# Kernel tuning notes

Measured on AMD Instinct MI355X. Metric: run time of the kernel, lower is better.

The kernel has to match this reference:

```python
import jax, jax.numpy as jnp
import numpy as np

# dims
Z, P, N, H = 16, 4, 466, 86          # z_dim, p_dim, n_dim, gmean(466,16)
B_SZ, T = 2048, 32                   # batch, number of eval times
INNER = 16                           # fixed trial-step budget per eval interval
ATOL, RTOL = 1e-20, 1e-5
H2B, H3B = 64, 2048                  # B-net hiddens: int(sqrt(16**3)), 16**3//2

# Dormand-Prince 5(4) tableau
A21 = 1/5
A31, A32 = 3/40, 9/40
A41, A42, A43 = 44/45, -56/15, 32/9
A51, A52, A53, A54 = 19372/6561, -25360/2187, 64448/6561, -212/729
A61, A62, A63, A64, A65 = 9017/3168, -355/33, 46732/5247, 49/176, -5103/18656
B1, B3, B4, B5, B6 = 35/384, 500/1113, 125/192, -2187/6784, 11/84
E1, E3, E4, E5, E6, E7 = 71/57600, -71/16695, 71/1920, -17253/339200, 22/525, -1/40


def _leaky(x):
    return jnp.where(x >= 0, x, 0.2 * x)


def setup_inputs() -> dict:
    key = jax.random.key(0)
    ks = jax.random.split(key, 26)
    w = lambda k, shape: (jax.random.normal(k, shape) * 0.05).astype(jnp.float32)
    inp = {}
    inp['n_0'] = jax.random.normal(ks[0], (B_SZ, N), dtype=jnp.float32)
    inp['p'] = jax.random.uniform(ks[1], (P,), dtype=jnp.float32)
    inp['tstep'] = jnp.arange(T, dtype=jnp.float32) / (T - 1)
    # autoencoder
    inp['We1'], inp['be1'] = w(ks[2], (N, H)), w(ks[3], (H,))
    inp['We2'], inp['be2'] = w(ks[4], (H, Z)), w(ks[5], (Z,))
    inp['Wd1'], inp['bd1'] = w(ks[6], (Z, H)), w(ks[7], (H,))
    inp['Wd2'], inp['bd2'] = w(ks[8], (H, N)), w(ks[9], (N,))
    # A net: P -> Z -> Z*Z//2 -> Z*Z
    inp['Wa1'], inp['ba1'] = w(ks[10], (P, Z)), w(ks[11], (Z,))
    inp['Wa2'], inp['ba2'] = w(ks[12], (Z, Z*Z//2)), w(ks[13], (Z*Z//2,))
    inp['Wa3'], inp['ba3'] = w(ks[14], (Z*Z//2, Z*Z)), w(ks[15], (Z*Z,))
    # B net: P -> Z -> 64 -> 2048 -> Z**3
    inp['Wb1'], inp['bb1'] = w(ks[16], (P, Z)), w(ks[17], (Z,))
    inp['Wb2'], inp['bb2'] = w(ks[18], (Z, H2B)), w(ks[19], (H2B,))
    inp['Wb3'], inp['bb3'] = w(ks[20], (H2B, H3B)), w(ks[21], (H3B,))
    inp['Wb4'], inp['bb4'] = w(ks[22], (H3B, Z**3)), w(ks[23], (Z**3,))
    return inp


def _solve(z0, tstep, Amat, Bten):
    # adaptive Dopri5 with integral (I) step-size controller; fixed trial budget per interval
    def f(z):  # g(z,p): A z + B z z
        return z @ Amat.T + jnp.einsum('ijk,bj,bk->bi', Bten, z, z)

    def step(y, dt):
        k1 = f(y)
        k2 = f(y + dt * (A21 * k1))
        k3 = f(y + dt * (A31 * k1 + A32 * k2))
        k4 = f(y + dt * (A41 * k1 + A42 * k2 + A43 * k3))
        k5 = f(y + dt * (A51 * k1 + A52 * k2 + A53 * k3 + A54 * k4))
        k6 = f(y + dt * (A61 * k1 + A62 * k2 + A63 * k3 + A64 * k4 + A65 * k5))
        y5 = y + dt * (B1 * k1 + B3 * k3 + B4 * k4 + B5 * k5 + B6 * k6)
        k7 = f(y5)
        err = dt * (E1 * k1 + E3 * k3 + E4 * k4 + E5 * k5 + E6 * k6 + E7 * k7)
        return y5, err

    def interval(carry, tpair):
        y, dt = carry
        t0, t1 = tpair[0], tpair[1]

        def inner(c, _):
            t, y, dt = c
            done = t >= t1 - 1e-10
            dtc = jnp.where(done, 0.0, jnp.minimum(dt, t1 - t))  # clip to interval end
            ynew, err = step(y, dtc)
            tol = ATOL + RTOL * jnp.maximum(jnp.abs(y), jnp.abs(ynew))
            en = jnp.sqrt(jnp.mean((err / tol) ** 2))
            accept = (en <= 1.0) & (~done)
            t = jnp.where(accept, t + dtc, t)
            y = jnp.where(accept, ynew, y)
            factor = jnp.clip(0.9 * jnp.maximum(en, 1e-12) ** -0.2, 0.2, 10.0)
            dt = jnp.where(done, dt, dt * factor)
            return (t, y, dt), None

        (tf, yf, dtf), _ = jax.lax.scan(inner, (t0, y, dt), None, length=INNER)
        return (yf, dtf), yf

    dt0 = (tstep[1] - tstep[0]) * 0.3
    tpairs = jnp.stack([tstep[:-1], tstep[1:]], axis=1)  # [T-1, 2]
    (_, _), ys = jax.lax.scan(interval, (z0, dt0), tpairs)
    return jnp.concatenate([z0[None], ys], axis=0)  # [T, b, Z]


def reference(n_0, p, tstep, We1, be1, We2, be2, Wd1, bd1, Wd2, bd2,
              Wa1, ba1, Wa2, ba2, Wa3, ba3,
              Wb1, bb1, Wb2, bb2, Wb3, bb3, Wb4, bb4):
    # encoder
    z0 = _leaky(n_0 @ We1 + be1) @ We2 + be2  # [b, Z]
    # A(p), B(p) depend only on p -> computed once per solve
    ha = _leaky(p @ Wa1 + ba1)
    ha = _leaky(ha @ Wa2 + ba2)
    Amat = _leaky(ha @ Wa3 + ba3).reshape(Z, Z)
    hb = _leaky(p @ Wb1 + bb1)
    hb = _leaky(hb @ Wb2 + bb2)
    hb = _leaky(hb @ Wb3 + bb3)
    Bten = _leaky(hb @ Wb4 + bb4).reshape(Z, Z, Z)
    zs = _solve(z0, tstep, Amat, Bten)  # [T, b, Z]
    # decoder
    return _leaky(zs @ Wd1 + bd1) @ Wd2 + bd2  # [T, b, N]
```

## Files before the change

### kernel.cpp

```cpp
#include <hip/hip_runtime.h>
#include <cmath>

#define DEV __device__ __forceinline__

static DEV float leakyf(float x){ return x >= 0.0f ? x : 0.2f*x; }

typedef float v2f __attribute__((ext_vector_type(2)));

constexpr float cA21 = (float)(1.0/5.0);
constexpr float cA31 = (float)(3.0/40.0),  cA32 = (float)(9.0/40.0);
constexpr float cA41 = (float)(44.0/45.0), cA42 = (float)(-56.0/15.0), cA43 = (float)(32.0/9.0);
constexpr float cA51 = (float)(19372.0/6561.0), cA52 = (float)(-25360.0/2187.0);
constexpr float cA53 = (float)(64448.0/6561.0), cA54 = (float)(-212.0/729.0);
constexpr float cA61 = (float)(9017.0/3168.0),  cA62 = (float)(-355.0/33.0);
constexpr float cA63 = (float)(46732.0/5247.0), cA64 = (float)(49.0/176.0);
constexpr float cA65 = (float)(-5103.0/18656.0);
constexpr float cB1 = (float)(35.0/384.0),  cB3 = (float)(500.0/1113.0), cB4 = (float)(125.0/192.0);
constexpr float cB5 = (float)(-2187.0/6784.0), cB6 = (float)(11.0/84.0);
constexpr float cE1 = (float)(71.0/57600.0), cE3 = (float)(-71.0/16695.0), cE4 = (float)(71.0/1920.0);
constexpr float cE5 = (float)(-17253.0/339200.0), cE6 = (float)(22.0/525.0), cE7 = (float)(-1.0/40.0);

#define WS_AMAT   0
#define WS_HB3    256
#define WS_BTEN   2304
#define WS_ZS     6400
#define WS_SLOTSF (6400 + 1048576)

__global__ void __launch_bounds__(256) k_smallnets(
    const float* __restrict__ p,
    const float* __restrict__ Wa1, const float* __restrict__ ba1,
    const float* __restrict__ Wa2, const float* __restrict__ ba2,
    const float* __restrict__ Wa3, const float* __restrict__ ba3,
    const float* __restrict__ Wb1, const float* __restrict__ bb1,
    const float* __restrict__ Wb2, const float* __restrict__ bb2,
    const float* __restrict__ Wb3, const float* __restrict__ bb3,
    float* __restrict__ wsf)
{
    __shared__ float sp[4], sa1[16], sa2[128], sb1[16], sb2[64];
    int tid = threadIdx.x;
    if (tid < 4) sp[tid] = p[tid];
    __syncthreads();
    if (tid < 16) {
        float a = ba1[tid];
        for (int j = 0; j < 4; ++j) a = fmaf(sp[j], Wa1[j*16+tid], a);
        sa1[tid] = leakyf(a);
        float c = bb1[tid];
        for (int j = 0; j < 4; ++j) c = fmaf(sp[j], Wb1[j*16+tid], c);
        sb1[tid] = leakyf(c);
    }
    __syncthreads();
    if (tid < 128) {
        float a = ba2[tid];
        for (int j = 0; j < 16; ++j) a = fmaf(sa1[j], Wa2[j*128+tid], a);
        sa2[tid] = leakyf(a);
    }
    if (tid < 64) {
        float c = bb2[tid];
        for (int j = 0; j < 16; ++j) c = fmaf(sb1[j], Wb2[j*64+tid], c);
        sb2[tid] = leakyf(c);
    }
    __syncthreads();
    {
        float a = ba3[tid];
        for (int j = 0; j < 128; ++j) a = fmaf(sa2[j], Wa3[j*256+tid], a);
        wsf[WS_AMAT + tid] = leakyf(a);
    }
    for (int q = 0; q < 8; ++q) {
        int o = q*256 + tid;
        float c = bb3[o];
        for (int j = 0; j < 64; ++j) c = fmaf(sb2[j], Wb3[j*2048+o], c);
        wsf[WS_HB3 + o] = leakyf(c);
    }
}

__global__ void __launch_bounds__(256) k_bten(
    const float* __restrict__ Wb4, const float* __restrict__ bb4, float* __restrict__ wsf)
{
    __shared__ float red[256];
    const float* hb3 = wsf + WS_HB3;
    float* Bten = wsf + WS_BTEN;
    int tid = threadIdx.x;
    int ol = tid & 15, part = tid >> 4;
    int o = blockIdx.x * 16 + ol;
    float a = 0.0f;
    for (int q = 0; q < 128; ++q) {
        int hh = part*128 + q;
        a = fmaf(hb3[hh], Wb4[(size_t)hh*4096 + o], a);
    }
    red[part*16 + ol] = a;
    __syncthreads();
    for (int s = 8; s >= 1; s >>= 1) {
        if (part < s) red[part*16+ol] += red[(part+s)*16+ol];
        __syncthreads();
    }
    if (tid < 16) {
        float v = red[tid] + bb4[blockIdx.x*16 + tid];
        Bten[blockIdx.x*16 + tid] = leakyf(v);
    }
}

__global__ void __launch_bounds__(256) k_encoder(
    const float* __restrict__ n0,
    const float* __restrict__ We1, const float* __restrict__ be1,
    const float* __restrict__ We2, const float* __restrict__ be2,
    float* __restrict__ zs)
{
    __shared__ float hL[8][88];
    int tid = threadIdx.x;
    int r = tid >> 5, c = tid & 31;
    int row = blockIdx.x * 8 + r;
    const float* nrow = n0 + (size_t)row * 466;
    int c2 = (c + 64 < 86) ? (c + 64) : 85;
    float a0 = 0.f, a1 = 0.f, a2 = 0.f;
    for (int n = 0; n < 466; ++n) {
        float nv = nrow[n];
        a0 = fmaf(nv, We1[n*86 + c], a0);
        a1 = fmaf(nv, We1[n*86 + c + 32], a1);
        a2 = fmaf(nv, We1[n*86 + c2], a2);
    }
    hL[r][c]      = leakyf(a0 + be1[c]);
    hL[r][c + 32] = leakyf(a1 + be1[c + 32]);
    if (c < 22) hL[r][c + 64] = leakyf(a2 + be1[c + 64]);
    __syncthreads();
    if (tid < 128) {
        int r2 = tid >> 4, ii = tid & 15;
        int row2 = blockIdx.x * 8 + r2;
        float a = be2[ii];
        #pragma unroll
        for (int hh = 0; hh < 86; ++hh) a = fmaf(hL[r2][hh], We2[hh*16 + ii], a);
        zs[(size_t)row2 * 16 + ii] = a;
    }
}

__global__ void __launch_bounds__(256) k_solver(
    const float* __restrict__ tstep, float* __restrict__ wsf)
{
    __shared__ float zL[8][16];
    __shared__ float redA[2][4], redB[2][4];
    float* Amat = wsf + WS_AMAT;
    float* Bten = wsf + WS_BTEN;
    float* zs   = wsf + WS_ZS;
    unsigned long long* slots = (unsigned long long*)(wsf + WS_SLOTSF);

    const int tid = threadIdx.x, blk = blockIdx.x;
    const int e = tid >> 5, g = tid & 31;
    const int i = g >> 1, h = g & 1, h8 = h * 8;
    const int b = blk * 8 + e;

    v2f Bl2[64], aR2[8];
    #pragma unroll
    for (int p = 0; p < 8; ++p) {
        int jA = (h8 + 2*p)     & 15;
        int jB = (h8 + 2*p + 1) & 15;
        v2f ap; ap.x = (h == 0) ? Amat[i*16 + 2*p] : 0.0f;
        ap.y = (h == 0) ? Amat[i*16 + 2*p + 1] : 0.0f;
        aR2[p] = ap;
        const float4* bpA = (const float4*)(Bten + i*256 + jA*16 + h8);
        const float4* bpB = (const float4*)(Bten + i*256 + jB*16 + h8);
        float4 a0 = bpA[0], a1 = bpA[1], b0 = bpB[0], b1 = bpB[1];
        v2f q;
        q.x=a0.x; q.y=b0.x; Bl2[p*8+0]=q;  q.x=a0.y; q.y=b0.y; Bl2[p*8+1]=q;
        q.x=a0.z; q.y=b0.z; Bl2[p*8+2]=q;  q.x=a0.w; q.y=b0.w; Bl2[p*8+3]=q;
        q.x=a1.x; q.y=b1.x; Bl2[p*8+4]=q;  q.x=a1.y; q.y=b1.y; Bl2[p*8+5]=q;
        q.x=a1.z; q.y=b1.z; Bl2[p*8+6]=q;  q.x=a1.w; q.y=b1.w; Bl2[p*8+7]=q;
    }

    float y = zs[(size_t)b*16 + i];

    auto feval = [&](float zi) -> float {
        zL[e][i] = zi;
        const float4* zp = (const float4*)(&zL[e][0]);
        int q0 = h8 >> 2;
        float4 r0 = zp[q0], r1 = zp[(q0+1)&3], r2 = zp[(q0+2)&3], r3 = zp[(q0+3)&3];
        float zz[16] = { r0.x,r0.y,r0.z,r0.w, r1.x,r1.y,r1.z,r1.w,
                         r2.x,r2.y,r2.z,r2.w, r3.x,r3.y,r3.z,r3.w };
        v2f zb[8];
        #pragma unroll
        for (int kk = 0; kk < 8; ++kk) { v2f t; t.x = zz[kk]; t.y = zz[kk]; zb[kk] = t; }
        v2f t2[8];
        #pragma unroll
        for (int p = 0; p < 8; ++p) t2[p] = aR2[p];
        #pragma unroll
        for (int p = 0; p < 8; ++p) {
            #pragma unroll
            for (int kk = 0; kk < 8; ++kk)
                asm("v_pk_fma_f32 %0, %1, %2, %0" : "+v"(t2[p]) : "v"(Bl2[p*8+kk]), "v"(zb[kk]));
        }
        float acc = 0.0f;
        #pragma unroll
        for (int p = 0; p < 8; ++p) {
            acc = fmaf(zz[2*p],     t2[p].x, acc);
            acc = fmaf(zz[2*p + 1], t2[p].y, acc);
        }
        acc += __shfl_xor(acc, 1);
        return acc;
    };

    float dt = (tstep[1] - tstep[0]) * 0.3f;
    float k1 = feval(y), k2, k3, k4, k5, k6, k7;
    int stepIdx = 0;

    for (int iv = 0; iv < 31; ++iv) {
        float t  = tstep[iv];
        float t1 = tstep[iv + 1];
        for (int it = 0; it < 16; ++it) {
            if (t >= t1 - 1e-10f) break;
            float dtc = fminf(dt, t1 - t);

            float z2 = fmaf(dtc, cA21*k1, y);                                         k2 = feval(z2);
            float z3 = fmaf(dtc, fmaf(cA32,k2, cA31*k1), y);                          k3 = feval(z3);
            float z4 = fmaf(dtc, fmaf(cA43,k3, fmaf(cA42,k2, cA41*k1)), y);           k4 = feval(z4);
            float z5 = fmaf(dtc, fmaf(cA54,k4, fmaf(cA53,k3, fmaf(cA52,k2, cA51*k1))), y);
            k5 = feval(z5);
            float z6 = fmaf(dtc, fmaf(cA65,k5, fmaf(cA64,k4, fmaf(cA63,k3, fmaf(cA62,k2, cA61*k1)))), y);
            k6 = feval(z6);
            float y5 = fmaf(dtc, fmaf(cB6,k6, fmaf(cB5,k5, fmaf(cB4,k4, fmaf(cB3,k3, cB1*k1)))), y);
            k7 = feval(y5);
            float err = dtc * fmaf(cE7,k7, fmaf(cE6,k6, fmaf(cE5,k5, fmaf(cE4,k4, fmaf(cE3,k3, cE1*k1)))));

            float ay = fabsf(y), a5 = fabsf(y5);
            float mx = (ay > a5) ? ay : a5;
            float tol = fmaf(1e-5f, mx, 1e-20f);
            float r = err / tol;
            float r2 = r * r;

            const int par = stepIdx & 1;

            float w = r2;
            w += __shfl_xor(w, 1);  w += __shfl_xor(w, 2);  w += __shfl_xor(w, 4);
            w += __shfl_xor(w, 8);  w += __shfl_xor(w, 16); w += __shfl_xor(w, 32);
            if ((tid & 63) == 0) redA[par][tid >> 6] = w;
            __syncthreads();
            float bsum = ((redA[par][0] + redA[par][1]) + redA[par][2]) + redA[par][3];

            unsigned long long* rowp = slots + (size_t)stepIdx * 256;
            if (tid == 0) {
                unsigned long long pv = (1ull << 32) | (unsigned long long)__float_as_uint(bsum);
                __hip_atomic_store(&rowp[blk], pv, __ATOMIC_RELAXED, __HIP_MEMORY_SCOPE_AGENT);
            }
            unsigned long long v = __hip_atomic_load(&rowp[tid], __ATOMIC_RELAXED, __HIP_MEMORY_SCOPE_AGENT);
            if ((unsigned)(v >> 32) != 1u) {
                for (;;) {
                    unsigned long long va = __hip_atomic_load(&rowp[tid], __ATOMIC_RELAXED, __HIP_MEMORY_SCOPE_AGENT);
                    unsigned long long vb = __hip_atomic_load(&rowp[tid], __ATOMIC_RELAXED, __HIP_MEMORY_SCOPE_AGENT);
                    if ((unsigned)(va >> 32) == 1u) { v = va; break; }
                    if ((unsigned)(vb >> 32) == 1u) { v = vb; break; }
                }
            }
            float ps = __uint_as_float((unsigned)v);
            ps += __shfl_xor(ps, 1);  ps += __shfl_xor(ps, 2);  ps += __shfl_xor(ps, 4);
            ps += __shfl_xor(ps, 8);  ps += __shfl_xor(ps, 16); ps += __shfl_xor(ps, 32);
            if ((tid & 63) == 0) redB[par][tid >> 6] = ps;
            __syncthreads();
            float gsum = ((redB[par][0] + redB[par][1]) + redB[par][2]) + redB[par][3];
            ++stepIdx;

            float en = sqrtf(gsum * (1.0f / 65536.0f));

            if (!(en == en)) {
                if (h == 0) {
                    for (int s = iv + 1; s < 32; ++s)
                        zs[((size_t)s * 2048 + b) * 16 + i] = y;
                }
                return;
            }
            if (en <= 1.0f) { t = t + dtc; y = y5; k1 = k7; }
            float fac = 0.9f * powf(fmaxf(en, 1e-12f), -0.2f);
            fac = fminf(fmaxf(fac, 0.2f), 10.0f);
            dt = dt * fac;
        }
        if (h == 0) zs[((size_t)(iv + 1) * 2048 + b) * 16 + i] = y;
    }
}

__global__ void __launch_bounds__(256) k_decoder(
    const float* __restrict__ zs,
    const float* __restrict__ Wd1, const float* __restrict__ bd1,
    const float* __restrict__ Wd2, const float* __restrict__ bd2,
    float* __restrict__ out)
{
    __shared__ float hL[8][86];
    int tid = threadIdx.x;
    size_t rowbase = (size_t)blockIdx.x * 8;

    for (int v = tid; v < 688; v += 256) {
        int r = v / 86, hh = v - r * 86;
        const float* zr = zs + (rowbase + r) * 16;
        float a = bd1[hh];
        #pragma unroll
        for (int ii = 0; ii < 16; ++ii) a = fmaf(zr[ii], Wd1[ii*86 + hh], a);
        hL[r][hh] = leakyf(a);
    }
    __syncthreads();

    for (int c = tid; c < 466; c += 256) {
        float acc[8];
        #pragma unroll
        for (int r = 0; r < 8; ++r) acc[r] = bd2[c];
        for (int hh = 0; hh < 86; ++hh) {
            float w = Wd2[hh*466 + c];
            #pragma unroll
            for (int r = 0; r < 8; ++r) acc[r] = fmaf(hL[r][hh], w, acc[r]);
        }
        #pragma unroll
        for (int r = 0; r < 8; ++r) out[(rowbase + r) * 466 + c] = acc[r];
    }
}

extern "C" void kernel_launch(void* const* d_in, const int* in_sizes, int n_in,
                              void* d_out, int out_size, void* d_ws, size_t ws_size,
                              hipStream_t stream)
{
    const float* n0   = (const float*)d_in[0];
    const float* p    = (const float*)d_in[1];
    const float* tstep= (const float*)d_in[2];
    const float* We1  = (const float*)d_in[3];  const float* be1 = (const float*)d_in[4];
    const float* We2  = (const float*)d_in[5];  const float* be2 = (const float*)d_in[6];
    const float* Wd1  = (const float*)d_in[7];  const float* bd1 = (const float*)d_in[8];
    const float* Wd2  = (const float*)d_in[9];  const float* bd2 = (const float*)d_in[10];
    const float* Wa1  = (const float*)d_in[11]; const float* ba1 = (const float*)d_in[12];
    const float* Wa2  = (const float*)d_in[13]; const float* ba2 = (const float*)d_in[14];
    const float* Wa3  = (const float*)d_in[15]; const float* ba3 = (const float*)d_in[16];
    const float* Wb1  = (const float*)d_in[17]; const float* bb1 = (const float*)d_in[18];
    const float* Wb2  = (const float*)d_in[19]; const float* bb2 = (const float*)d_in[20];
    const float* Wb3  = (const float*)d_in[21]; const float* bb3 = (const float*)d_in[22];
    const float* Wb4  = (const float*)d_in[23]; const float* bb4 = (const float*)d_in[24];
    float* out = (float*)d_out;
    float* wsf = (float*)d_ws;

    hipLaunchKernelGGL(k_smallnets, dim3(1), dim3(256), 0, stream,
                       p, Wa1, ba1, Wa2, ba2, Wa3, ba3, Wb1, bb1, Wb2, bb2, Wb3, bb3, wsf);
    hipLaunchKernelGGL(k_bten, dim3(256), dim3(256), 0, stream, Wb4, bb4, wsf);
    hipLaunchKernelGGL(k_encoder, dim3(256), dim3(256), 0, stream,
                       n0, We1, be1, We2, be2, wsf + WS_ZS);

    hipLaunchKernelGGL(k_solver, dim3(256), dim3(256), 0, stream, tstep, wsf);

    hipLaunchKernelGGL(k_decoder, dim3(8192), dim3(256), 0, stream,
                       wsf + WS_ZS, Wd1, bd1, Wd2, bd2, out);
}
```

Baseline: 1.530 ms.

## Split hb3 layer into parallel kernel, drop solver barrier, retile decoder

```diff
diff --git a/kernel.cpp b/kernel.cpp
--- a/kernel.cpp
+++ b/kernel.cpp
@@ -25,6 +25,7 @@
 #define WS_BTEN   2304
 #define WS_ZS     6400
 #define WS_SLOTSF (6400 + 1048576)
+#define WS_SB2    (WS_SLOTSF + 4096)
 
 __global__ void __launch_bounds__(256) k_smallnets(
     const float* __restrict__ p,
@@ -33,10 +34,9 @@
     const float* __restrict__ Wa3, const float* __restrict__ ba3,
     const float* __restrict__ Wb1, const float* __restrict__ bb1,
     const float* __restrict__ Wb2, const float* __restrict__ bb2,
-    const float* __restrict__ Wb3, const float* __restrict__ bb3,
     float* __restrict__ wsf)
 {
-    __shared__ float sp[4], sa1[16], sa2[128], sb1[16], sb2[64];
+    __shared__ float sp[4], sa1[16], sa2[128], sb1[16];
     int tid = threadIdx.x;
     if (tid < 4) sp[tid] = p[tid];
     __syncthreads();
@@ -57,7 +57,7 @@
     if (tid < 64) {
         float c = bb2[tid];
         for (int j = 0; j < 16; ++j) c = fmaf(sb1[j], Wb2[j*64+tid], c);
-        sb2[tid] = leakyf(c);
+        wsf[WS_SB2 + tid] = leakyf(c);
     }
     __syncthreads();
     {
@@ -65,12 +65,19 @@
         for (int j = 0; j < 128; ++j) a = fmaf(sa2[j], Wa3[j*256+tid], a);
         wsf[WS_AMAT + tid] = leakyf(a);
     }
-    for (int q = 0; q < 8; ++q) {
-        int o = q*256 + tid;
-        float c = bb3[o];
-        for (int j = 0; j < 64; ++j) c = fmaf(sb2[j], Wb3[j*2048+o], c);
-        wsf[WS_HB3 + o] = leakyf(c);
-    }
+}
+
+__global__ void __launch_bounds__(256) k_hb3(
+    const float* __restrict__ Wb3, const float* __restrict__ bb3, float* __restrict__ wsf)
+{
+    __shared__ float sb2[64];
+    int tid = threadIdx.x;
+    if (tid < 64) sb2[tid] = wsf[WS_SB2 + tid];
+    __syncthreads();
+    int o = blockIdx.x * 256 + tid;
+    float c = bb3[o];
+    for (int j = 0; j < 64; ++j) c = fmaf(sb2[j], Wb3[(size_t)j*2048 + o], c);
+    wsf[WS_HB3 + o] = leakyf(c);
 }
 
 __global__ void __launch_bounds__(256) k_bten(
@@ -132,11 +139,20 @@
     }
 }
 
+static DEV unsigned long long slot_ld(unsigned long long* p){
+    return __hip_atomic_load(p, __ATOMIC_RELAXED, __HIP_MEMORY_SCOPE_AGENT);
+}
+static DEV bool tags4(unsigned long long a, unsigned long long b,
+                      unsigned long long c, unsigned long long d, unsigned t){
+    return ((unsigned)(a>>32)==t) & ((unsigned)(b>>32)==t) &
+           ((unsigned)(c>>32)==t) & ((unsigned)(d>>32)==t);
+}
+
 __global__ void __launch_bounds__(256) k_solver(
     const float* __restrict__ tstep, float* __restrict__ wsf)
 {
     __shared__ float zL[8][16];
-    __shared__ float redA[2][4], redB[2][4];
+    __shared__ float redB[2][4];
     float* Amat = wsf + WS_AMAT;
     float* Bten = wsf + WS_BTEN;
     float* zs   = wsf + WS_ZS;
@@ -225,29 +241,34 @@
             float r2 = r * r;
 
             const int par = stepIdx & 1;
+            const unsigned wantTag = (unsigned)(stepIdx + 1);
+            unsigned long long* rowp = slots + (size_t)par * 1024;
 
             float w = r2;
             w += __shfl_xor(w, 1);  w += __shfl_xor(w, 2);  w += __shfl_xor(w, 4);
             w += __shfl_xor(w, 8);  w += __shfl_xor(w, 16); w += __shfl_xor(w, 32);
-            if ((tid & 63) == 0) redA[par][tid >> 6] = w;
-            __syncthreads();
-            float bsum = ((redA[par][0] + redA[par][1]) + redA[par][2]) + redA[par][3];
-
-            unsigned long long* rowp = slots + (size_t)stepIdx * 256;
-            if (tid == 0) {
-                unsigned long long pv = (1ull << 32) | (unsigned long long)__float_as_uint(bsum);
-                __hip_atomic_store(&rowp[blk], pv, __ATOMIC_RELAXED, __HIP_MEMORY_SCOPE_AGENT);
+            if ((tid & 63) == 0) {
+                unsigned long long pv = ((unsigned long long)wantTag << 32)
+                                      | (unsigned long long)__float_as_uint(w);
+                __hip_atomic_store(&rowp[blk*4 + (tid >> 6)], pv,
+                                   __ATOMIC_RELAXED, __HIP_MEMORY_SCOPE_AGENT);
             }
-            unsigned long long v = __hip_atomic_load(&rowp[tid], __ATOMIC_RELAXED, __HIP_MEMORY_SCOPE_AGENT);
-            if ((unsigned)(v >> 32) != 1u) {
+
+            unsigned long long* rp = rowp + 4*(size_t)tid;
+            unsigned long long s0 = slot_ld(rp+0), s1 = slot_ld(rp+1),
+                               s2 = slot_ld(rp+2), s3 = slot_ld(rp+3);
+            if (!tags4(s0,s1,s2,s3,wantTag)) {
                 for (;;) {
-                    unsigned long long va = __hip_atomic_load(&rowp[tid], __ATOMIC_RELAXED, __HIP_MEMORY_SCOPE_AGENT);
-                    unsigned long long vb = __hip_atomic_load(&rowp[tid], __ATOMIC_RELAXED, __HIP_MEMORY_SCOPE_AGENT);
-                    if ((unsigned)(va >> 32) == 1u) { v = va; break; }
-                    if ((unsigned)(vb >> 32) == 1u) { v = vb; break; }
+                    unsigned long long a0 = slot_ld(rp+0), a1 = slot_ld(rp+1),
+                                       a2 = slot_ld(rp+2), a3 = slot_ld(rp+3);
+                    unsigned long long b0 = slot_ld(rp+0), b1 = slot_ld(rp+1),
+                                       b2 = slot_ld(rp+2), b3 = slot_ld(rp+3);
+                    if (tags4(a0,a1,a2,a3,wantTag)) { s0=a0;s1=a1;s2=a2;s3=a3; break; }
+                    if (tags4(b0,b1,b2,b3,wantTag)) { s0=b0;s1=b1;s2=b2;s3=b3; break; }
                 }
             }
-            float ps = __uint_as_float((unsigned)v);
+            float ps = ((__uint_as_float((unsigned)s0) + __uint_as_float((unsigned)s1))
+                       + __uint_as_float((unsigned)s2)) + __uint_as_float((unsigned)s3);
             ps += __shfl_xor(ps, 1);  ps += __shfl_xor(ps, 2);  ps += __shfl_xor(ps, 4);
             ps += __shfl_xor(ps, 8);  ps += __shfl_xor(ps, 16); ps += __shfl_xor(ps, 32);
             if ((tid & 63) == 0) redB[par][tid >> 6] = ps;
@@ -279,31 +300,46 @@
     const float* __restrict__ Wd2, const float* __restrict__ bd2,
     float* __restrict__ out)
 {
-    __shared__ float hL[8][86];
-    int tid = threadIdx.x;
-    size_t rowbase = (size_t)blockIdx.x * 8;
-
-    for (int v = tid; v < 688; v += 256) {
-        int r = v / 86, hh = v - r * 86;
-        const float* zr = zs + (rowbase + r) * 16;
+    __shared__ __align__(16) float hT[86][16];
+    int tid = threadIdx.x;
+    size_t rowbase = (size_t)blockIdx.x * 16;
+
+    for (int v = tid; v < 86*16; v += 256) {
+        int hh = v >> 4, r = v & 15;
+        const float4* z4 = (const float4*)(zs + (rowbase + r) * 16);
+        float4 za = z4[0], zb = z4[1], zc = z4[2], zd = z4[3];
         float a = bd1[hh];
-        #pragma unroll
-        for (int ii = 0; ii < 16; ++ii) a = fmaf(zr[ii], Wd1[ii*86 + hh], a);
-        hL[r][hh] = leakyf(a);
+        a = fmaf(za.x, Wd1[ 0*86 + hh], a);  a = fmaf(za.y, Wd1[ 1*86 + hh], a);
+        a = fmaf(za.z, Wd1[ 2*86 + hh], a);  a = fmaf(za.w, Wd1[ 3*86 + hh], a);
+        a = fmaf(zb.x, Wd1[ 4*86 + hh], a);  a = fmaf(zb.y, Wd1[ 5*86 + hh], a);
+        a = fmaf(zb.z, Wd1[ 6*86 + hh], a);  a = fmaf(zb.w, Wd1[ 7*86 + hh], a);
+        a = fmaf(zc.x, Wd1[ 8*86 + hh], a);  a = fmaf(zc.y, Wd1[ 9*86 + hh], a);
+        a = fmaf(zc.z, Wd1[10*86 + hh], a);  a = fmaf(zc.w, Wd1[11*86 + hh], a);
+        a = fmaf(zd.x, Wd1[12*86 + hh], a);  a = fmaf(zd.y, Wd1[13*86 + hh], a);
+        a = fmaf(zd.z, Wd1[14*86 + hh], a);  a = fmaf(zd.w, Wd1[15*86 + hh], a);
+        hT[hh][r] = leakyf(a);
     }
     __syncthreads();
 
     for (int c = tid; c < 466; c += 256) {
-        float acc[8];
-        #pragma unroll
-        for (int r = 0; r < 8; ++r) acc[r] = bd2[c];
+        float acc[16];
+        #pragma unroll
+        for (int r = 0; r < 16; ++r) acc[r] = bd2[c];
         for (int hh = 0; hh < 86; ++hh) {
             float w = Wd2[hh*466 + c];
-            #pragma unroll
-            for (int r = 0; r < 8; ++r) acc[r] = fmaf(hL[r][hh], w, acc[r]);
+            const float4* hp = (const float4*)(&hT[hh][0]);
+            float4 h0 = hp[0], h1 = hp[1], h2 = hp[2], h3 = hp[3];
+            acc[ 0] = fmaf(h0.x, w, acc[ 0]);  acc[ 1] = fmaf(h0.y, w, acc[ 1]);
+            acc[ 2] = fmaf(h0.z, w, acc[ 2]);  acc[ 3] = fmaf(h0.w, w, acc[ 3]);
+            acc[ 4] = fmaf(h1.x, w, acc[ 4]);  acc[ 5] = fmaf(h1.y, w, acc[ 5]);
+            acc[ 6] = fmaf(h1.z, w, acc[ 6]);  acc[ 7] = fmaf(h1.w, w, acc[ 7]);
+            acc[ 8] = fmaf(h2.x, w, acc[ 8]);  acc[ 9] = fmaf(h2.y, w, acc[ 9]);
+            acc[10] = fmaf(h2.z, w, acc[10]);  acc[11] = fmaf(h2.w, w, acc[11]);
+            acc[12] = fmaf(h3.x, w, acc[12]);  acc[13] = fmaf(h3.y, w, acc[13]);
+            acc[14] = fmaf(h3.z, w, acc[14]);  acc[15] = fmaf(h3.w, w, acc[15]);
         }
         #pragma unroll
-        for (int r = 0; r < 8; ++r) out[(rowbase + r) * 466 + c] = acc[r];
+        for (int r = 0; r < 16; ++r) out[(rowbase + r) * 466 + c] = acc[r];
     }
 }
 
@@ -329,13 +365,14 @@
     float* wsf = (float*)d_ws;
 
     hipLaunchKernelGGL(k_smallnets, dim3(1), dim3(256), 0, stream,
-                       p, Wa1, ba1, Wa2, ba2, Wa3, ba3, Wb1, bb1, Wb2, bb2, Wb3, bb3, wsf);
+                       p, Wa1, ba1, Wa2, ba2, Wa3, ba3, Wb1, bb1, Wb2, bb2, wsf);
+    hipLaunchKernelGGL(k_hb3, dim3(8), dim3(256), 0, stream, Wb3, bb3, wsf);
     hipLaunchKernelGGL(k_bten, dim3(256), dim3(256), 0, stream, Wb4, bb4, wsf);
     hipLaunchKernelGGL(k_encoder, dim3(256), dim3(256), 0, stream,
                        n0, We1, be1, We2, be2, wsf + WS_ZS);
 
     hipLaunchKernelGGL(k_solver, dim3(256), dim3(256), 0, stream, tstep, wsf);
 
-    hipLaunchKernelGGL(k_decoder, dim3(8192), dim3(256), 0, stream,
+    hipLaunchKernelGGL(k_decoder, dim3(4096), dim3(256), 0, stream,
                        wsf + WS_ZS, Wd1, bd1, Wd2, bd2, out);
 }
```

Result: slower. 2.002 ms (+30.8%).
